# Kernel tuning notes

Hardware: AMD Instinct MI355X
Metric: run time of the kernel (lower is better)

The kernel has to match this reference:

```python
import jax, jax.numpy as jnp
import numpy as np

H, HK, HD = 6, 2, 128  # n_heads, n_kv_heads, head_dim (from AcousticTransformerArgs defaults)


def setup_inputs() -> dict:
    key = jax.random.key(0)
    k1, k2, k3, k4, k5 = jax.random.split(key, 5)
    B, S, D = 2, 4096, 768
    s = 0.02
    return {
        "x": jax.random.normal(k1, (B, S, D), dtype=jnp.float32),
        "wq": jax.random.normal(k2, (H * HD, D), dtype=jnp.float32) * s,
        "wk": jax.random.normal(k3, (HK * HD, D), dtype=jnp.float32) * s,
        "wv": jax.random.normal(k4, (HK * HD, D), dtype=jnp.float32) * s,
        "wo": jax.random.normal(k5, (D, H * HD), dtype=jnp.float32) * s,
    }


def reference(x, wq, wk, wv, wo):
    B, S, D = x.shape
    rep = H // HK  # GQA repeat factor (3)
    scale = 1.0 / jnp.sqrt(jnp.asarray(HD, x.dtype))
    # projections (torch Linear: y = x @ W^T)
    q = (x @ wq.T).reshape(B, S, HK, rep, HD) * scale  # head h = g*rep + r
    k = (x @ wk.T).reshape(B, S, HK, HD)
    v = (x @ wv.T).reshape(B, S, HK, HD)
    # bidirectional (no mask) attention with GQA broadcast instead of physical repeat
    scores = jnp.einsum("bsgrd,btgd->bgrst", q, k)  # [B,HK,rep,S,S]
    attn = jax.nn.softmax(scores, axis=-1)
    out = jnp.einsum("bgrst,btgd->bsgrd", attn, v).reshape(B, S, H * HD)
    return out @ wo.T
```

## Files before the change

### kernel.cpp

```cpp
#include <hip/hip_runtime.h>
#include <hip/hip_bf16.h>
#include <type_traits>

using bf16 = __hip_bfloat16;
typedef __attribute__((ext_vector_type(8))) short bf16x8;
typedef __attribute__((ext_vector_type(4))) float floatx4;

static constexpr int Bb = 2, S = 4096, D = 768, H = 6, HK = 2, HD = 128, REP = 3;
static constexpr int M_ROWS = Bb * S;
static constexpr int NQKV = 1280;

__device__ __forceinline__ floatx4 mfma16(bf16x8 a, bf16x8 b, floatx4 c) {
  return __builtin_amdgcn_mfma_f32_16x16x32_bf16(a, b, c, 0, 0, 0);
}

__device__ __forceinline__ void gld_lds16(const bf16* g, bf16* l) {
  __builtin_amdgcn_global_load_lds(
      (const __attribute__((address_space(1))) unsigned int*)g,
      (__attribute__((address_space(3))) unsigned int*)l, 16, 0, 0);
}

#if defined(__has_builtin)
#if __has_builtin(__builtin_amdgcn_exp2f)
#define EXP2F(x) __builtin_amdgcn_exp2f(x)
#endif
#endif
#ifndef EXP2F
#define EXP2F(x) exp2f(x)
#endif

__device__ __forceinline__ unsigned pk2(float a, float b) {
  unsigned ua = __builtin_bit_cast(unsigned, a) + 0x8000u;
  unsigned ub = __builtin_bit_cast(unsigned, b) + 0x8000u;
#if defined(__has_builtin) && __has_builtin(__builtin_amdgcn_perm)
  return __builtin_amdgcn_perm(ub, ua, 0x07060302);
#else
  return (ua >> 16) | (ub & 0xffff0000u);
#endif
}

__device__ __forceinline__ void perm32swap(unsigned& a, unsigned& b) {
  asm volatile("v_permlane32_swap_b32 %0, %1" : "+v"(a), "+v"(b));
}
__device__ __forceinline__ void perm16swap(unsigned& a, unsigned& b) {
  asm volatile("v_permlane16_swap_b32 %0, %1" : "+v"(a), "+v"(b));
}

static constexpr size_t E_X  = (size_t)M_ROWS * D;
static constexpr size_t E_WQ = E_X + (size_t)H * HD * D;
static constexpr size_t E_WK = E_WQ + (size_t)HK * HD * D;
static constexpr size_t E_WV = E_WK + (size_t)HK * HD * D;
static constexpr size_t E_WO = E_WV + (size_t)D * H * HD;

__global__ __launch_bounds__(256) void cvt_all(const float* __restrict__ x,
                                               const float* __restrict__ wq,
                                               const float* __restrict__ wk,
                                               const float* __restrict__ wv,
                                               const float* __restrict__ wo,
                                               bf16* __restrict__ xb,
                                               bf16* __restrict__ wqkvb,
                                               bf16* __restrict__ wob, float qscale) {
  size_t i = ((size_t)blockIdx.x * 256 + threadIdx.x) * 4;
  const float* src;
  bf16* dst;
  float s = 1.f;
  size_t off;
  if (i < E_X)        { src = x;  dst = xb;                 off = i; }
  else if (i < E_WQ)  { src = wq; dst = wqkvb;              off = i - E_X; s = qscale; }
  else if (i < E_WK)  { src = wk; dst = wqkvb + 589824;     off = i - E_WQ; }
  else if (i < E_WV)  { src = wv; dst = wqkvb + 786432;     off = i - E_WK; }
  else                { src = wo; dst = wob;                off = i - E_WV; }
  float4 v = *(const float4*)(src + off);
  uint2 st;
  st.x = pk2(v.x * s, v.y * s);
  st.y = pk2(v.z * s, v.w * s);
  *(uint2*)(dst + off) = st;
}

__global__ __launch_bounds__(256, 3) void gemm_qkv(const bf16* __restrict__ A,
                                                   const bf16* __restrict__ W,
                                                   bf16* __restrict__ C,
                                                   bf16* __restrict__ Vt,
                                                   int M, int N, int K) {
  const int tid = threadIdx.x;
  const int wave = tid >> 6, lane = tid & 63;
  const int quad = lane >> 4, lq = lane & 15;
  const int m0 = blockIdx.x * 128, n0 = blockIdx.y * 128;
  const int wm = (wave & 1) * 64, wn = (wave >> 1) * 64;

  __shared__ __align__(16) bf16 As[128 * 64];
  __shared__ __align__(16) bf16 Ws[128 * 64];

  floatx4 acc[4][4] = {};

  const int srow = lane >> 3, sc = lane & 7;

  if (n0 < 1024) {
    for (int k0 = 0; k0 < K; k0 += 64) {
#pragma unroll
      for (int i = 0; i < 4; ++i) {
        int ig = wave * 4 + i;
        int r = ig * 8 + srow;
        int c = sc ^ (r & 7);
        gld_lds16(&A[(size_t)(m0 + r) * K + k0 + c * 8], &As[ig * 512]);
        gld_lds16(&W[(size_t)(n0 + r) * K + k0 + c * 8], &Ws[ig * 512]);
      }
      __syncthreads();
#pragma unroll
      for (int kh = 0; kh < 2; ++kh) {
        bf16x8 af[4], wf[4];
#pragma unroll
        for (int i = 0; i < 4; ++i) {
          int ra = wm + i * 16 + lq, rw = wn + i * 16 + lq;
          af[i] = *(const bf16x8*)&As[ra * 64 + (((kh * 4 + quad) ^ (ra & 7)) * 8)];
          wf[i] = *(const bf16x8*)&Ws[rw * 64 + (((kh * 4 + quad) ^ (rw & 7)) * 8)];
        }
#pragma unroll
        for (int i = 0; i < 4; ++i)
#pragma unroll
          for (int j = 0; j < 4; ++j) acc[i][j] = mfma16(wf[j], af[i], acc[i][j]);
      }
      __syncthreads();
    }
#pragma unroll
    for (int i = 0; i < 4; ++i)
#pragma unroll
      for (int j = 0; j < 4; ++j) {
        uint2 st;
        st.x = pk2(acc[i][j][0], acc[i][j][1]);
        st.y = pk2(acc[i][j][2], acc[i][j][3]);
        int row = m0 + wm + i * 16 + lq;
        int col = n0 + wn + j * 16 + quad * 4;
        *(uint2*)&C[(size_t)row * N + col] = st;
      }
    return;
  }

  for (int k0 = 0; k0 < K; k0 += 64) {
#pragma unroll
    for (int i = 0; i < 4; ++i) {
      int ig = wave * 4 + i;
      int r = ig * 8 + srow;
      int c = sc ^ (r & 7);
      gld_lds16(&A[(size_t)(m0 + r) * K + k0 + c * 8], &As[ig * 512]);
      gld_lds16(&W[(size_t)(n0 + r) * K + k0 + c * 8], &Ws[ig * 512]);
    }
    __syncthreads();
#pragma unroll
    for (int kh = 0; kh < 2; ++kh) {
      bf16x8 af[4], wf[4];
#pragma unroll
      for (int i = 0; i < 4; ++i) {
        int ra = wm + i * 16 + lq, rw = wn + i * 16 + lq;
        af[i] = *(const bf16x8*)&As[ra * 64 + (((kh * 4 + quad) ^ (ra & 7)) * 8)];
        wf[i] = *(const bf16x8*)&Ws[rw * 64 + (((kh * 4 + quad) ^ (rw & 7)) * 8)];
      }
#pragma unroll
      for (int i = 0; i < 4; ++i)
#pragma unroll
        for (int j = 0; j < 4; ++j) acc[i][j] = mfma16(af[i], wf[j], acc[i][j]);
    }
    __syncthreads();
  }

  bf16* tb = (wave < 2 ? As : Ws) + (wave & 1) * 4096;
  char* tc = (char*)tb;
#pragma unroll
  for (int i = 0; i < 4; ++i)
#pragma unroll
    for (int j = 0; j < 4; ++j) {
      uint2 st;
      st.x = pk2(acc[i][j][0], acc[i][j][1]);
      st.y = pk2(acc[i][j][2], acc[i][j][3]);
      int col = j * 16 + lq;
      int cc = (i * 2 + (quad >> 1)) ^ (col & 7);
      *(uint2*)(tc + col * 128 + cc * 16 + (quad & 1) * 8) = st;
    }
  const int b = m0 >> 12;
  const int dd_off = lane >> 3, schunk = lane & 7;
  const int sbase = (m0 & 4095) + wm + schunk * 8;
#pragma unroll
  for (int e = 0; e < 8; ++e) {
    int cl = e * 8 + dd_off;
    int col = (n0 - 1024) + wn + cl;
    int gg = col >> 7, dd = col & 127;
    bf16x8 vv = *(const bf16x8*)(tc + cl * 128 + ((schunk ^ (cl & 7)) * 16));
    *(bf16x8*)&Vt[((size_t)(b * HK + gg) * HD + dd) * S + sbase] = vv;
  }
}

__global__ __launch_bounds__(256, 3) void gemm_out(const bf16* __restrict__ A,
                                                   const bf16* __restrict__ W,
                                                   float* __restrict__ C,
                                                   int M, int N, int K) {
  const int tid = threadIdx.x;
  const int wave = tid >> 6, lane = tid & 63;
  const int quad = lane >> 4, lq = lane & 15;
  const int m0 = blockIdx.x * 128, n0 = blockIdx.y * 64;
  const int wm = (wave & 1) * 64, wn = (wave >> 1) * 32;

  __shared__ __align__(16) bf16 As[128 * 64];
  __shared__ __align__(16) bf16 Ws[64 * 64];

  floatx4 acc[4][2] = {};

  const int srow = lane >> 3, sc = lane & 7;

  for (int k0 = 0; k0 < K; k0 += 64) {
#pragma unroll
    for (int i = 0; i < 4; ++i) {
      int ig = wave * 4 + i;
      int r = ig * 8 + srow;
      int c = sc ^ (r & 7);
      gld_lds16(&A[(size_t)(m0 + r) * K + k0 + c * 8], &As[ig * 512]);
    }
#pragma unroll
    for (int i = 0; i < 2; ++i) {
      int ig = wave * 2 + i;
      int r = ig * 8 + srow;
      int c = sc ^ (r & 7);
      gld_lds16(&W[(size_t)(n0 + r) * K + k0 + c * 8], &Ws[ig * 512]);
    }
    __syncthreads();
#pragma unroll
    for (int kh = 0; kh < 2; ++kh) {
      bf16x8 af[4], wf[2];
#pragma unroll
      for (int i = 0; i < 4; ++i) {
        int ra = wm + i * 16 + lq;
        af[i] = *(const bf16x8*)&As[ra * 64 + (((kh * 4 + quad) ^ (ra & 7)) * 8)];
      }
#pragma unroll
      for (int j = 0; j < 2; ++j) {
        int rw = wn + j * 16 + lq;
        wf[j] = *(const bf16x8*)&Ws[rw * 64 + (((kh * 4 + quad) ^ (rw & 7)) * 8)];
      }
#pragma unroll
      for (int i = 0; i < 4; ++i)
#pragma unroll
        for (int j = 0; j < 2; ++j) acc[i][j] = mfma16(wf[j], af[i], acc[i][j]);
    }
    __syncthreads();
  }
#pragma unroll
  for (int i = 0; i < 4; ++i)
#pragma unroll
    for (int j = 0; j < 2; ++j) {
      int row = m0 + wm + i * 16 + lq;
      int col = n0 + wn + j * 16 + quad * 4;
      *(floatx4*)&C[(size_t)row * N + col] = acc[i][j];
    }
}

__global__ __launch_bounds__(256, 2) void flash_attn(const bf16* __restrict__ QKV,
                                                     const bf16* __restrict__ Vt,
                                                     bf16* __restrict__ O) {
  const int bid = blockIdx.x;
  const int bg = (bid & 7) >> 1;
  const int b = bg >> 1, g = bg & 1;
  const int qt = ((bid >> 3) << 1) | (bid & 1);
  const int q0 = qt * 32;

  const int tid = threadIdx.x;
  const int w = tid >> 6, lane = tid & 63;
  const int half = w >> 1, wp = w & 1;
  const int quad = lane >> 4, lq = lane & 15;

  __shared__ __align__(16) char smem[81920];
  bf16* Ks = (bf16*)smem;
  bf16* Vs = (bf16*)(smem + 32768);

  const bf16* Kgh = QKV + (size_t)b * S * NQKV + H * HD + g * HD + (size_t)half * 2048 * NQKV;
  const bf16* Vgh = Vt + (size_t)(b * HK + g) * HD * S + half * 2048;

  auto stage = [&](int t0, int kbuf, int vbuf) {
    bf16* kd = Ks + (kbuf * 2 + half) * 4096;
    bf16* vd = Vs + (vbuf * 2 + half) * 4096;
#pragma unroll
    for (int i = 0; i < 4; ++i) {
      int ig = wp * 4 + i;
      int tl = ig * 4 + (lane >> 4);
      int c = (lane & 15) ^ (tl & 15);
      gld_lds16(Kgh + (size_t)(t0 + tl) * NQKV + c * 8, kd + ig * 512);
    }
#pragma unroll
    for (int i = 0; i < 4; ++i) {
      int ig = wp * 4 + i;
      int dl = ig * 16 + (lane >> 2);
      int c = (lane & 3) ^ ((dl >> 1) & 3);
      gld_lds16(Vgh + (size_t)dl * S + t0 + c * 8, vd + ig * 512);
    }
  };

  stage(0, 0, 0);

  const bf16* Qg = QKV + ((size_t)b * S + q0 + wp * 16 + lq) * NQKV + g * REP * HD;
  bf16x8 qf[3][4];
#pragma unroll
  for (int u = 0; u < 3; ++u)
#pragma unroll
    for (int kk = 0; kk < 4; ++kk)
      qf[u][kk] = *(const bf16x8*)(Qg + u * HD + kk * 32 + quad * 8);

  bf16x8 ones;
#pragma unroll
  for (int j = 0; j < 8; ++j) ones[j] = (short)0x3F80;

  floatx4 o[3][8] = {};
  floatx4 lacc[3] = {};
  bf16x8 pf_prev[3];
  const int sw = (lq >> 1) & 3;

#pragma unroll 2
  for (int it = 0; it < 64; ++it) {
    const int kcur = it & 1;
    __syncthreads();
    if (it + 1 < 64) stage((it + 1) * 32, kcur ^ 1, (it + 1) % 3);

    const bf16* ks = Ks + (kcur * 2 + half) * 4096;

    floatx4 sf[3][2] = {};
    __builtin_amdgcn_s_setprio(1);
#pragma unroll
    for (int tt = 0; tt < 2; ++tt)
#pragma unroll
      for (int kk = 0; kk < 4; ++kk) {
        int c = (kk * 4 + quad) ^ lq;
        bf16x8 kf = *(const bf16x8*)&ks[(tt * 16 + lq) * 128 + c * 8];
#pragma unroll
        for (int u = 0; u < 3; ++u) sf[u][tt] = mfma16(kf, qf[u][kk], sf[u][tt]);
      }

    if (it) {
      const bf16* vs = Vs + ((((it - 1) % 3) * 2) + half) * 4096;
#pragma unroll
      for (int u = 0; u < 3; ++u) lacc[u] = mfma16(ones, pf_prev[u], lacc[u]);
#pragma unroll
      for (int dd = 0; dd < 8; ++dd) {
        bf16x8 vf = *(const bf16x8*)&vs[(dd * 16 + lq) * 32 + ((quad ^ sw) * 8)];
#pragma unroll
        for (int u = 0; u < 3; ++u) o[u][dd] = mfma16(vf, pf_prev[u], o[u][dd]);
      }
    }
    __builtin_amdgcn_s_setprio(0);

#pragma unroll
    for (int u = 0; u < 3; ++u) {
      unsigned A0 = pk2(EXP2F(sf[u][0][0]), EXP2F(sf[u][0][1]));
      unsigned A1 = pk2(EXP2F(sf[u][0][2]), EXP2F(sf[u][0][3]));
      unsigned B0 = pk2(EXP2F(sf[u][1][0]), EXP2F(sf[u][1][1]));
      unsigned B1 = pk2(EXP2F(sf[u][1][2]), EXP2F(sf[u][1][3]));
      perm32swap(A0, B0);
      perm16swap(A0, B0);
      perm32swap(A1, B1);
      perm16swap(A1, B1);
      union { unsigned d[4]; bf16x8 v; } pu;
      pu.d[0] = A0; pu.d[1] = A1; pu.d[2] = B0; pu.d[3] = B1;
      pf_prev[u] = pu.v;
    }
  }

  {
    const bf16* vs = Vs + (0 * 2 + half) * 4096;
#pragma unroll
    for (int u = 0; u < 3; ++u) lacc[u] = mfma16(ones, pf_prev[u], lacc[u]);
#pragma unroll
    for (int dd = 0; dd < 8; ++dd) {
      bf16x8 vf = *(const bf16x8*)&vs[(dd * 16 + lq) * 32 + ((quad ^ sw) * 8)];
#pragma unroll
      for (int u = 0; u < 3; ++u) o[u][dd] = mfma16(vf, pf_prev[u], o[u][dd]);
    }
  }

  __syncthreads();
  floatx4* oscr = (floatx4*)smem;
  float* lscr = (float*)(smem + 49152);
  if (half == 1) {
#pragma unroll
    for (int u = 0; u < 3; ++u) {
#pragma unroll
      for (int dd = 0; dd < 8; ++dd)
        oscr[((wp * 3 + u) * 8 + dd) * 64 + lane] = o[u][dd];
      lscr[(wp * 3 + u) * 64 + lane] = lacc[u][0];
    }
  }
  __syncthreads();
  if (half == 0) {
    const size_t row = (size_t)b * S + q0 + wp * 16 + lq;
#pragma unroll
    for (int u = 0; u < 3; ++u) {
      float l = lacc[u][0] + lscr[(wp * 3 + u) * 64 + lane];
      float rinv = 1.0f / l;
#pragma unroll
      for (int dd = 0; dd < 8; ++dd) {
        floatx4 oc = o[u][dd] + oscr[((wp * 3 + u) * 8 + dd) * 64 + lane];
        uint2 st;
        st.x = pk2(oc[0] * rinv, oc[1] * rinv);
        st.y = pk2(oc[2] * rinv, oc[3] * rinv);
        int col = (g * REP + u) * HD + dd * 16 + quad * 4;
        *(uint2*)&O[row * (H * HD) + col] = st;
      }
    }
  }
}

static inline size_t al256(size_t x) { return (x + 255) & ~size_t(255); }

extern "C" void kernel_launch(void* const* d_in, const int* in_sizes, int n_in,
                              void* d_out, int out_size, void* d_ws, size_t ws_size,
                              hipStream_t stream) {
  const float* x  = (const float*)d_in[0];
  const float* wq = (const float*)d_in[1];
  const float* wk = (const float*)d_in[2];
  const float* wv = (const float*)d_in[3];
  const float* wo = (const float*)d_in[4];
  float* out = (float*)d_out;

  char* w = (char*)d_ws;
  size_t off = 0;
  auto carve = [&](size_t elems) {
    bf16* p = (bf16*)(w + off);
    off = al256(off + elems * sizeof(bf16));
    return p;
  };
  bf16* xb    = carve((size_t)M_ROWS * D);
  bf16* wqkvb = carve((size_t)NQKV * D);
  bf16* wob   = carve((size_t)D * (H * HD));
  bf16* QKVb  = carve((size_t)M_ROWS * NQKV);
  bf16* Vtb   = carve((size_t)M_ROWS * (HK * HD));
  bf16* Ab    = carve((size_t)M_ROWS * (H * HD));

  const float qscale = 0.1275174465f;

  cvt_all<<<(int)(E_WO / 1024), 256, 0, stream>>>(x, wq, wk, wv, wo, xb, wqkvb, wob, qscale);

  gemm_qkv<<<dim3(M_ROWS / 128, NQKV / 128), 256, 0, stream>>>(
      xb, wqkvb, QKVb, Vtb, M_ROWS, NQKV, D);

  flash_attn<<<512, 256, 0, stream>>>(QKVb, Vtb, Ab);

  gemm_out<<<dim3(M_ROWS / 128, D / 64), 256, 0, stream>>>(
      Ab, wob, out, M_ROWS, D, H * HD);
}
```

Baseline: 222.7 us.

## Fuse fp32-to-bf16 conversion of x into QKV GEMM A-tile loading

Result: slower. 360.3 us (+61.8%).

```diff
diff --git a/kernel.cpp b/kernel.cpp
--- a/kernel.cpp
+++ b/kernel.cpp
@@ -46,30 +46,26 @@
   asm volatile("v_permlane16_swap_b32 %0, %1" : "+v"(a), "+v"(b));
 }
 
-static constexpr size_t E_X  = (size_t)M_ROWS * D;
-static constexpr size_t E_WQ = E_X + (size_t)H * HD * D;
-static constexpr size_t E_WK = E_WQ + (size_t)HK * HD * D;
-static constexpr size_t E_WV = E_WK + (size_t)HK * HD * D;
-static constexpr size_t E_WO = E_WV + (size_t)D * H * HD;
-
-__global__ __launch_bounds__(256) void cvt_all(const float* __restrict__ x,
-                                               const float* __restrict__ wq,
-                                               const float* __restrict__ wk,
-                                               const float* __restrict__ wv,
-                                               const float* __restrict__ wo,
-                                               bf16* __restrict__ xb,
-                                               bf16* __restrict__ wqkvb,
-                                               bf16* __restrict__ wob, float qscale) {
+static constexpr size_t W_WQ = (size_t)H * HD * D;
+static constexpr size_t W_WK = W_WQ + (size_t)HK * HD * D;
+static constexpr size_t W_WV = W_WK + (size_t)HK * HD * D;
+static constexpr size_t W_WO = W_WV + (size_t)D * H * HD;
+
+__global__ __launch_bounds__(256) void cvt_w(const float* __restrict__ wq,
+                                             const float* __restrict__ wk,
+                                             const float* __restrict__ wv,
+                                             const float* __restrict__ wo,
+                                             bf16* __restrict__ wqkvb,
+                                             bf16* __restrict__ wob, float qscale) {
   size_t i = ((size_t)blockIdx.x * 256 + threadIdx.x) * 4;
   const float* src;
   bf16* dst;
   float s = 1.f;
   size_t off;
-  if (i < E_X)        { src = x;  dst = xb;                 off = i; }
-  else if (i < E_WQ)  { src = wq; dst = wqkvb;              off = i - E_X; s = qscale; }
-  else if (i < E_WK)  { src = wk; dst = wqkvb + 589824;     off = i - E_WQ; }
-  else if (i < E_WV)  { src = wv; dst = wqkvb + 786432;     off = i - E_WK; }
-  else                { src = wo; dst = wob;                off = i - E_WV; }
+  if (i < W_WQ)       { src = wq; dst = wqkvb;              off = i; s = qscale; }
+  else if (i < W_WK)  { src = wk; dst = wqkvb + 589824;     off = i - W_WQ; }
+  else if (i < W_WV)  { src = wv; dst = wqkvb + 786432;     off = i - W_WK; }
+  else                { src = wo; dst = wob;                off = i - W_WV; }
   float4 v = *(const float4*)(src + off);
   uint2 st;
   st.x = pk2(v.x * s, v.y * s);
@@ -77,7 +73,7 @@
   *(uint2*)(dst + off) = st;
 }
 
-__global__ __launch_bounds__(256, 3) void gemm_qkv(const bf16* __restrict__ A,
+__global__ __launch_bounds__(256, 3) void gemm_qkv(const float* __restrict__ X,
                                                    const bf16* __restrict__ W,
                                                    bf16* __restrict__ C,
                                                    bf16* __restrict__ Vt,
@@ -94,34 +90,70 @@
   floatx4 acc[4][4] = {};
 
   const int srow = lane >> 3, sc = lane & 7;
-
-  if (n0 < 1024) {
-    for (int k0 = 0; k0 < K; k0 += 64) {
+  const int ar = tid >> 1, cb = (tid & 1) * 4;
+
+  const float* Ag = X + (size_t)(m0 + ar) * K + (tid & 1) * 32;
+
+  float4 pf[8];
+  auto loadA = [&](int k0) {
+#pragma unroll
+    for (int j = 0; j < 8; ++j) pf[j] = *(const float4*)(Ag + k0 + j * 4);
+  };
+  auto writeA = [&]() {
+#pragma unroll
+    for (int t = 0; t < 4; ++t) {
+      int c = cb + t;
+      uint4 st;
+      st.x = pk2(pf[2 * t].x, pf[2 * t].y);
+      st.y = pk2(pf[2 * t].z, pf[2 * t].w);
+      st.z = pk2(pf[2 * t + 1].x, pf[2 * t + 1].y);
+      st.w = pk2(pf[2 * t + 1].z, pf[2 * t + 1].w);
+      *(uint4*)&As[ar * 64 + ((c ^ (ar & 7)) * 8)] = st;
+    }
+  };
+  auto stageW = [&](int k0) {
+#pragma unroll
+    for (int i = 0; i < 4; ++i) {
+      int ig = wave * 4 + i;
+      int r = ig * 8 + srow;
+      int c = sc ^ (r & 7);
+      gld_lds16(&W[(size_t)(n0 + r) * K + k0 + c * 8], &Ws[ig * 512]);
+    }
+  };
+
+  loadA(0);
+
+  const bool qk = (n0 < 1024);
+  for (int k0 = 0; k0 < K; k0 += 64) {
+    writeA();
+    stageW(k0);
+    __syncthreads();
+    if (k0 + 64 < K) loadA(k0 + 64);
+#pragma unroll
+    for (int kh = 0; kh < 2; ++kh) {
+      bf16x8 af[4], wf[4];
 #pragma unroll
       for (int i = 0; i < 4; ++i) {
-        int ig = wave * 4 + i;
-        int r = ig * 8 + srow;
-        int c = sc ^ (r & 7);
-        gld_lds16(&A[(size_t)(m0 + r) * K + k0 + c * 8], &As[ig * 512]);
-        gld_lds16(&W[(size_t)(n0 + r) * K + k0 + c * 8], &Ws[ig * 512]);
-      }
-      __syncthreads();
-#pragma unroll
-      for (int kh = 0; kh < 2; ++kh) {
-        bf16x8 af[4], wf[4];
-#pragma unroll
-        for (int i = 0; i < 4; ++i) {
-          int ra = wm + i * 16 + lq, rw = wn + i * 16 + lq;
-          af[i] = *(const bf16x8*)&As[ra * 64 + (((kh * 4 + quad) ^ (ra & 7)) * 8)];
-          wf[i] = *(const bf16x8*)&Ws[rw * 64 + (((kh * 4 + quad) ^ (rw & 7)) * 8)];
-        }
+        int ra = wm + i * 16 + lq, rw = wn + i * 16 + lq;
+        af[i] = *(const bf16x8*)&As[ra * 64 + (((kh * 4 + quad) ^ (ra & 7)) * 8)];
+        wf[i] = *(const bf16x8*)&Ws[rw * 64 + (((kh * 4 + quad) ^ (rw & 7)) * 8)];
+      }
+      if (qk) {
 #pragma unroll
         for (int i = 0; i < 4; ++i)
 #pragma unroll
           for (int j = 0; j < 4; ++j) acc[i][j] = mfma16(wf[j], af[i], acc[i][j]);
-      }
-      __syncthreads();
-    }
+      } else {
+#pragma unroll
+        for (int i = 0; i < 4; ++i)
+#pragma unroll
+          for (int j = 0; j < 4; ++j) acc[i][j] = mfma16(af[i], wf[j], acc[i][j]);
+      }
+    }
+    __syncthreads();
+  }
+
+  if (qk) {
 #pragma unroll
     for (int i = 0; i < 4; ++i)
 #pragma unroll
@@ -134,33 +166,6 @@
         *(uint2*)&C[(size_t)row * N + col] = st;
       }
     return;
-  }
-
-  for (int k0 = 0; k0 < K; k0 += 64) {
-#pragma unroll
-    for (int i = 0; i < 4; ++i) {
-      int ig = wave * 4 + i;
-      int r = ig * 8 + srow;
-      int c = sc ^ (r & 7);
-      gld_lds16(&A[(size_t)(m0 + r) * K + k0 + c * 8], &As[ig * 512]);
-      gld_lds16(&W[(size_t)(n0 + r) * K + k0 + c * 8], &Ws[ig * 512]);
-    }
-    __syncthreads();
-#pragma unroll
-    for (int kh = 0; kh < 2; ++kh) {
-      bf16x8 af[4], wf[4];
-#pragma unroll
-      for (int i = 0; i < 4; ++i) {
-        int ra = wm + i * 16 + lq, rw = wn + i * 16 + lq;
-        af[i] = *(const bf16x8*)&As[ra * 64 + (((kh * 4 + quad) ^ (ra & 7)) * 8)];
-        wf[i] = *(const bf16x8*)&Ws[rw * 64 + (((kh * 4 + quad) ^ (rw & 7)) * 8)];
-      }
-#pragma unroll
-      for (int i = 0; i < 4; ++i)
-#pragma unroll
-        for (int j = 0; j < 4; ++j) acc[i][j] = mfma16(af[i], wf[j], acc[i][j]);
-    }
-    __syncthreads();
   }
 
   bf16* tb = (wave < 2 ? As : Ws) + (wave & 1) * 4096;
@@ -423,7 +428,6 @@
     off = al256(off + elems * sizeof(bf16));
     return p;
   };
-  bf16* xb    = carve((size_t)M_ROWS * D);
   bf16* wqkvb = carve((size_t)NQKV * D);
   bf16* wob   = carve((size_t)D * (H * HD));
   bf16* QKVb  = carve((size_t)M_ROWS * NQKV);
@@ -432,10 +436,10 @@
 
   const float qscale = 0.1275174465f;
 
-  cvt_all<<<(int)(E_WO / 1024), 256, 0, stream>>>(x, wq, wk, wv, wo, xb, wqkvb, wob, qscale);
+  cvt_w<<<(int)(W_WO / 1024), 256, 0, stream>>>(wq, wk, wv, wo, wqkvb, wob, qscale);
 
   gemm_qkv<<<dim3(M_ROWS / 128, NQKV / 128), 256, 0, stream>>>(
-      xb, wqkvb, QKVb, Vtb, M_ROWS, NQKV, D);
+      x, wqkvb, QKVb, Vtb, M_ROWS, NQKV, D);
 
   flash_attn<<<512, 256, 0, stream>>>(QKVb, Vtb, Ab);
 
```
